# Kernel tuning notes

Hardware: AMD Instinct MI355X
Metric: run time of the kernel (lower is better)

The kernel has to match this reference:

```python
import jax, jax.numpy as jnp
import numpy as np


def setup_inputs() -> dict:
    key = jax.random.key(0)
    k0, k1, k2, k3 = jax.random.split(key, 4)
    B, H, W, C, h = 2, 64, 64, 256, 8
    N = H * W
    # per-pixel, per-head (dy, dx) match offsets; a few pixels of displacement
    max_offset = jax.random.normal(k0, (B, N, h, 2), dtype=jnp.float32) * 4.0
    q = jax.random.normal(k1, (B, N, C), dtype=jnp.float32)
    k = jax.random.normal(k2, (B, N, C), dtype=jnp.float32)
    v = jax.random.normal(k3, (B, N, C), dtype=jnp.float32)
    return {"max_offset": max_offset, "q": q, "k": k, "v": v,
            "H": H, "W": W, "r_h": 3, "r_w": 3}


def reference(max_offset, q, k, v, H, W, r_h, r_w):
    """MatchAttention fused forward (l1_norm, scale=1.0).

    Each query pixel (y,x), head g attends to a (2*r_h+1)x(2*r_w+1) window
    centered at (y,x) + round(max_offset[...,g]), clamped to the image.
    Similarity is the negative L1 distance between q and gathered k.
    Returns (output [B,N,C], attn_out [B,N,h,K]).
    """
    B, N, C = q.shape
    h = max_offset.shape[2]
    Ch = C // h
    scale = 1.0
    attn_type = "l1_norm"  # fixed; 'l2_norm' would use squared distance

    # window deltas, K = (2*r_h+1)*(2*r_w+1)
    dy = jnp.arange(-r_h, r_h + 1)
    dx = jnp.arange(-r_w, r_w + 1)
    gy, gx = jnp.meshgrid(dy, dx, indexing="ij")
    ddy, ddx = gy.reshape(-1), gx.reshape(-1)  # [K]

    ys = (jnp.arange(N) // W)[None, :, None]  # [1,N,1]
    xs = (jnp.arange(N) % W)[None, :, None]

    off = jnp.round(max_offset).astype(jnp.int32)  # [B,N,h,2] (dy,dx)
    cy = ys + off[..., 0]                          # [B,N,h] window center
    cx = xs + off[..., 1]
    py = jnp.clip(cy[..., None] + ddy, 0, H - 1)   # [B,N,h,K]
    px = jnp.clip(cx[..., None] + ddx, 0, W - 1)
    idx = py * W + px                              # flat pixel index, [B,N,h,K]

    # split heads and move head axis forward: [B,h,N,Ch]
    qh = q.reshape(B, N, h, Ch).transpose(0, 2, 1, 3)
    kh = k.reshape(B, N, h, Ch).transpose(0, 2, 1, 3)
    vh = v.reshape(B, N, h, Ch).transpose(0, 2, 1, 3)
    idx_t = idx.transpose(0, 2, 1, 3)              # [B,h,N,K]

    # gather windows: [B,h,N,K,Ch]
    gather = jax.vmap(jax.vmap(lambda tbl, i: tbl[i]))
    kg = gather(kh, idx_t)
    vg = gather(vh, idx_t)

    # negative L1 distance similarity, softmax over window
    sim = -scale * jnp.abs(qh[:, :, :, None, :] - kg).sum(-1)  # [B,h,N,K]
    attn = jax.nn.softmax(sim, axis=-1)

    out = jnp.einsum("bhnk,bhnkc->bhnc", attn, vg)
    output = out.transpose(0, 2, 1, 3).reshape(B, N, C)
    attn_out = attn.transpose(0, 2, 1, 3)          # [B,N,h,K]
    return output, attn_out
```

## Files before the change

### kernel.cpp

```cpp
#include <hip/hip_runtime.h>
#include <hip/hip_fp16.h>
#include <math.h>

constexpr int B = 2, H = 64, W = 64, C = 256, NH = 8, CH = 32;
constexpr int R = 3, KW = 7, KK = 49, N = H * W;
constexpr int PIX = 32;

template <int CTRL>
static __device__ __forceinline__ float dpp_mov(float v) {
  union { float f; int i; } u;
  u.f = v;
  u.i = __builtin_amdgcn_update_dpp(u.i, u.i, CTRL, 0xf, 0xf, true);
  return u.f;
}
#define DPP_QUAD_XOR1 0xB1
#define DPP_QUAD_XOR2 0x4E
#define DPP_HALF_MIRROR 0x141

__global__ void __launch_bounds__(256) pack_kv_kernel(
    const float* __restrict__ kp, const float* __restrict__ vp,
    __half* __restrict__ kv) {
  const int idx = blockIdx.x * 256 + threadIdx.x;
  const int e8 = idx & 7;
  const int g = (idx >> 3) & 7;
  const int bn = idx >> 6;
  const float4 kf = *(const float4*)(kp + (size_t)bn * C + g * CH + e8 * 4);
  const float4 vf = *(const float4*)(vp + (size_t)bn * C + g * CH + e8 * 4);
  __half2 o[4];
  o[0] = __floats2half2_rn(kf.x, kf.y);
  o[1] = __floats2half2_rn(kf.z, kf.w);
  o[2] = __floats2half2_rn(vf.x, vf.y);
  o[3] = __floats2half2_rn(vf.z, vf.w);
  *(float4*)(kv + ((size_t)(bn * NH + g) * 64 + e8 * 8)) = *(float4*)o;
}

__global__ void __launch_bounds__(256, 2) match_attn_kernel(
    const float* __restrict__ moff, const float* __restrict__ qp,
    const __half* __restrict__ kvp, float* __restrict__ outp,
    float* __restrict__ attnp) {
  const int t = threadIdx.x;
  const int e8 = t & 7;
  const int p = t >> 3;

  const int xcd = blockIdx.x & 7;
  const int rest = blockIdx.x >> 3;
  const int bg = xcd * 2 + (rest >> 7);
  const int slot = rest & 127;
  const int y = slot >> 1;
  const int x = (slot & 1) * PIX + p;
  const int g = bg & 7;
  const int b = bg >> 3;
  const int n = y * W + x;

  const float2 off = *(const float2*)(moff + ((size_t)(b * N + n) * NH + g) * 2);
  const int cy = y + (int)rintf(off.x);
  const int cx = x + (int)rintf(off.y);

  int pxo[KW], rowo[KW];
#pragma unroll
  for (int i = 0; i < KW; ++i) {
    pxo[i] = min(max(cx + i - R, 0), W - 1) << 10;
    rowo[i] = min(max(cy + i - R, 0), H - 1) << 16;
  }
  const char* kvimg = (const char*)kvp +
      (size_t)b * N * NH * 128 + g * 128 + e8 * 16;

  const int chn = g * CH + e8 * 4;
  const float4 q0 = *(const float4*)(qp + (size_t)(b * N + n) * C + chn);
  const __half2 q01 = __floats2half2_rn(q0.x, q0.y);
  const __half2 q23 = __floats2half2_rn(q0.z, q0.w);

  float ev7[KW];
#pragma unroll
  for (int i = 0; i < KW; ++i) ev7[i] = 0.f;
  float4 acc = {0.f, 0.f, 0.f, 0.f};
  float d0 = 0.f, d1 = 0.f;

  union KV { float4 f; __half2 h[4]; };
  for (int iy = 0; iy < KW; ++iy) {
    const int ro = rowo[iy];
    KV kv[KW];
#pragma unroll
    for (int ix = 0; ix < KW; ++ix)
      kv[ix].f = *(const float4*)(kvimg + (ro + pxo[ix]));

    const bool own = (iy == e8);
#pragma unroll
    for (int ix = 0; ix < KW; ++ix) {
      const __half2 d01h = __habs2(__hsub2(q01, kv[ix].h[0]));
      const __half2 d23h = __habs2(__hsub2(q23, kv[ix].h[1]));
      const float2 f01 = __half22float2(d01h);
      const float2 f23 = __half22float2(d23h);
      float s = (f01.x + f01.y) + (f23.x + f23.y);
      s += dpp_mov<DPP_QUAD_XOR1>(s);
      s += dpp_mov<DPP_QUAD_XOR2>(s);
      s += dpp_mov<DPP_HALF_MIRROR>(s);
      const float e = __expf(-s);
      if (ix & 1) d1 += e; else d0 += e;
      if (own) ev7[ix] = e;
      const float2 v01 = __half22float2(kv[ix].h[2]);
      const float2 v23 = __half22float2(kv[ix].h[3]);
      acc.x += e * v01.x; acc.y += e * v01.y;
      acc.z += e * v23.x; acc.w += e * v23.y;
    }
  }
  const float inv = 1.0f / (d0 + d1);

  float4 o;
  o.x = acc.x * inv; o.y = acc.y * inv; o.z = acc.z * inv; o.w = acc.w * inv;
  *(float4*)(outp + (size_t)(b * N + n) * C + chn) = o;

  if (e8 < KW) {
    float* attn_row = attnp + ((size_t)(b * N + n) * NH + g) * KK + e8 * KW;
#pragma unroll
    for (int ix = 0; ix < KW; ++ix) attn_row[ix] = ev7[ix] * inv;
  }
}

extern "C" void kernel_launch(void* const* d_in, const int* in_sizes, int n_in,
                              void* d_out, int out_size, void* d_ws, size_t ws_size,
                              hipStream_t stream) {
  const float* moff = (const float*)d_in[0];
  const float* q    = (const float*)d_in[1];
  const float* k    = (const float*)d_in[2];
  const float* v    = (const float*)d_in[3];
  float* out  = (float*)d_out;
  float* attn = out + (size_t)B * N * C;
  __half* kv = (__half*)d_ws;

  pack_kv_kernel<<<B * N * NH * 8 / 256, 256, 0, stream>>>(k, v, kv);
  const int grid = B * NH * N / PIX;
  match_attn_kernel<<<grid, 256, 0, stream>>>(moff, q, kv, out, attn);
}
```

Measured before the change: 116.2 us.

## Double-buffer KV window rows into LDS via async global_load_lds

Replaces the per-row direct global loads of packed K/V with async global-to-LDS copies into a per-wave double buffer. The next window row is prefetched while the current one is computed, with manual waitcnt management. The occupancy hint of two blocks per SM is dropped. This adds LDS traffic and 56KB of shared memory per block, which limits occupancy, and the hand-coded waitcnt values risk subtle ordering errors.

```diff
diff --git a/kernel.cpp b/kernel.cpp
--- a/kernel.cpp
+++ b/kernel.cpp
@@ -17,6 +17,11 @@
 #define DPP_QUAD_XOR2 0x4E
 #define DPP_HALF_MIRROR 0x141
 
+#define GLD16(gaddr, laddr)                                                   \
+  __builtin_amdgcn_global_load_lds(                                           \
+      (const __attribute__((address_space(1))) void*)(gaddr),                 \
+      (__attribute__((address_space(3))) void*)(laddr), 16, 0, 0)
+
 __global__ void __launch_bounds__(256) pack_kv_kernel(
     const float* __restrict__ kp, const float* __restrict__ vp,
     __half* __restrict__ kv) {
@@ -34,13 +39,19 @@
   *(float4*)(kv + ((size_t)(bn * NH + g) * 64 + e8 * 8)) = *(float4*)o;
 }
 
-__global__ void __launch_bounds__(256, 2) match_attn_kernel(
+__global__ void __launch_bounds__(256) match_attn_kernel(
     const float* __restrict__ moff, const float* __restrict__ qp,
     const __half* __restrict__ kvp, float* __restrict__ outp,
     float* __restrict__ attnp) {
+  __shared__ __align__(16) char smem[4][2][KW * 1024];
+
   const int t = threadIdx.x;
   const int e8 = t & 7;
   const int p = t >> 3;
+  const int wv = t >> 6;
+  const int lane16 = (t & 63) * 16;
+  char* buf0 = &smem[wv][0][0];
+  char* buf1 = &smem[wv][1][0];
 
   const int xcd = blockIdx.x & 7;
   const int rest = blockIdx.x >> 3;
@@ -76,19 +87,31 @@
   float4 acc = {0.f, 0.f, 0.f, 0.f};
   float d0 = 0.f, d1 = 0.f;
 
+#pragma unroll
+  for (int ix = 0; ix < KW; ++ix)
+    GLD16(kvimg + (rowo[0] + pxo[ix]), buf0 + (ix << 10));
+
   union KV { float4 f; __half2 h[4]; };
+#pragma unroll
   for (int iy = 0; iy < KW; ++iy) {
-    const int ro = rowo[iy];
-    KV kv[KW];
+    char* cur = (iy & 1) ? buf1 : buf0;
+    char* nxt = (iy & 1) ? buf0 : buf1;
+    if (iy + 1 < KW) {
+      __builtin_amdgcn_s_waitcnt(0xC07F);
 #pragma unroll
-    for (int ix = 0; ix < KW; ++ix)
-      kv[ix].f = *(const float4*)(kvimg + (ro + pxo[ix]));
-
+      for (int ix = 0; ix < KW; ++ix)
+        GLD16(kvimg + (rowo[iy + 1] + pxo[ix]), nxt + (ix << 10));
+      __builtin_amdgcn_s_waitcnt(0x0F77);
+    } else {
+      __builtin_amdgcn_s_waitcnt(0x0F70);
+    }
     const bool own = (iy == e8);
 #pragma unroll
     for (int ix = 0; ix < KW; ++ix) {
-      const __half2 d01h = __habs2(__hsub2(q01, kv[ix].h[0]));
-      const __half2 d23h = __habs2(__hsub2(q23, kv[ix].h[1]));
+      KV kv;
+      kv.f = *(const float4*)(cur + (ix << 10) + lane16);
+      const __half2 d01h = __habs2(__hsub2(q01, kv.h[0]));
+      const __half2 d23h = __habs2(__hsub2(q23, kv.h[1]));
       const float2 f01 = __half22float2(d01h);
       const float2 f23 = __half22float2(d23h);
       float s = (f01.x + f01.y) + (f23.x + f23.y);
@@ -98,8 +121,8 @@
       const float e = __expf(-s);
       if (ix & 1) d1 += e; else d0 += e;
       if (own) ev7[ix] = e;
-      const float2 v01 = __half22float2(kv[ix].h[2]);
-      const float2 v23 = __half22float2(kv[ix].h[3]);
+      const float2 v01 = __half22float2(kv.h[2]);
+      const float2 v23 = __half22float2(kv.h[3]);
       acc.x += e * v01.x; acc.y += e * v01.y;
       acc.z += e * v23.x; acc.w += e * v23.y;
     }
```

Result: slower. 121.0 us (+4.1%).
